# Performance work log

Hardware: AMD Instinct MI355X
Metric: run time of the kernel (lower is better)

Reference implementation:

```python
import jax, jax.numpy as jnp
import numpy as np

HIDDEN = 2048
N_HEADS = 16
HEAD_DIM = HIDDEN // N_HEADS
ROPE_THETA = 10000.0
BSZ, SEQ = 2, 2048
NEG_INF = -1e9


def setup_inputs() -> dict:
    key = jax.random.key(0)
    ks = jax.random.split(key, 5)
    scale = 1.0 / np.sqrt(HIDDEN)
    hidden_states = jax.random.normal(ks[0], (BSZ, SEQ, HIDDEN), dtype=jnp.float32)
    Wq = jax.random.normal(ks[1], (HIDDEN, HIDDEN), dtype=jnp.float32) * scale
    Wk = jax.random.normal(ks[2], (HIDDEN, HIDDEN), dtype=jnp.float32) * scale
    Wv = jax.random.normal(ks[3], (HIDDEN, HIDDEN), dtype=jnp.float32) * scale
    Wo = jax.random.normal(ks[4], (HIDDEN, HIDDEN), dtype=jnp.float32) * scale
    # additive causal mask, [1, 1, S, S]
    causal = jnp.triu(jnp.full((SEQ, SEQ), NEG_INF, dtype=jnp.float32), k=1)
    attention_mask = causal[None, None, :, :]
    position_ids = jnp.arange(SEQ, dtype=jnp.int32)
    return {
        "hidden_states": hidden_states,
        "Wq": Wq, "Wk": Wk, "Wv": Wv, "Wo": Wo,
        "attention_mask": attention_mask,
        "position_ids": position_ids,
    }


def _rotate_half(x):
    half = x.shape[-1] // 2
    return jnp.concatenate((-x[..., half:], x[..., :half]), axis=-1)


def _rope_tables(seq_len, position_ids):
    # inv_freq: [head_dim/2]
    inv_freq = 1.0 / (ROPE_THETA ** (jnp.arange(0, HEAD_DIM, 2, dtype=jnp.float32) / HEAD_DIM))
    t = jnp.arange(seq_len, dtype=jnp.float32)
    freqs = t[:, None] * inv_freq[None, :]              # [S, D/2]
    emb = jnp.concatenate((freqs, freqs), axis=-1)      # [S, D]
    cos = jnp.cos(emb)[position_ids]                    # [S, D]
    sin = jnp.sin(emb)[position_ids]
    return cos, sin


def reference(hidden_states, Wq, Wk, Wv, Wo, attention_mask, position_ids):
    b, s, h = hidden_states.shape
    def proj(W):
        return (hidden_states @ W.T).reshape(b, s, N_HEADS, HEAD_DIM).transpose(0, 2, 1, 3)
    q = proj(Wq)  # [B, H, S, D]
    k = proj(Wk)
    v = proj(Wv)
    cos, sin = _rope_tables(s, position_ids)            # [S, D], broadcasts over B,H
    q = q * cos + _rotate_half(q) * sin
    k = k * cos + _rotate_half(k) * sin
    scores = jnp.einsum('bhqd,bhkd->bhqk', q, k) / np.sqrt(HEAD_DIM)
    scores = scores + attention_mask
    w = jax.nn.softmax(scores, axis=-1)
    out = jnp.einsum('bhqk,bhkd->bhqd', w, v)           # [B, H, S, D]
    out = out.transpose(0, 2, 1, 3).reshape(b, s, h)
    return out @ Wo.T
```

## Files before the change

kernel.cpp:

```cpp
#include <hip/hip_runtime.h>
#include <cstdint>
#include <cstddef>

typedef __bf16 bf16;
typedef __bf16 bf16x4 __attribute__((ext_vector_type(4)));
typedef __bf16 bf16x8 __attribute__((ext_vector_type(8)));
typedef float  f32x4  __attribute__((ext_vector_type(4)));

#define HIDDEN 2048
#define NHEADS 16
#define HDIM   128
#define BSZ    2
#define SEQ    2048
#define BS     (BSZ*SEQ)
#define QKW    (2*HIDDEN)

__device__ __forceinline__ void async16(const bf16* g, bf16* l) {
    __builtin_amdgcn_global_load_lds(
        (const __attribute__((address_space(1))) unsigned int*)g,
        (__attribute__((address_space(3))) unsigned int*)l, 16, 0, 0);
}

__global__ __launch_bounds__(256) void cast_all(const float* __restrict__ hs,
                                                const float* __restrict__ Wq,
                                                const float* __restrict__ Wk,
                                                const float* __restrict__ Wv,
                                                const float* __restrict__ Wo,
                                                bf16* __restrict__ hs_b,
                                                bf16* __restrict__ wqkv,
                                                bf16* __restrict__ wo_b) {
    int i = blockIdx.x * 256 + threadIdx.x;
    const float* src; bf16* dst; int off;
    if (i < 2097152) { src = hs; dst = hs_b; off = i; }
    else {
        int j = i - 2097152;
        int r = j >> 20;
        off = j & 1048575;
        if      (r == 0) { src = Wq; dst = wqkv; }
        else if (r == 1) { src = Wk; dst = wqkv + (size_t)4194304; }
        else if (r == 2) { src = Wv; dst = wqkv + (size_t)8388608; }
        else             { src = Wo; dst = wo_b; }
    }
    const float4 v = ((const float4*)src)[off];
    bf16x4 o;
    o.x = (bf16)v.x; o.y = (bf16)v.y; o.z = (bf16)v.z; o.w = (bf16)v.w;
    ((bf16x4*)dst)[off] = o;
}

__global__ __launch_bounds__(256) void rope_table(const int* __restrict__ pos,
                                                  float2* __restrict__ tab) {
    int i = blockIdx.x * 256 + threadIdx.x;
    int s = i >> 6, p = i & 63;
    float t = (float)pos[s];
    float inv = expf(-(float)(2 * p) * (9.2103403719761836f / 128.0f));
    float sn, cs;
    sincosf(t * inv, &sn, &cs);
    tab[i] = make_float2(cs, sn);
}

__global__ __launch_bounds__(256) void gemm_qkv(const bf16* __restrict__ A,
                                                const bf16* __restrict__ Bt,
                                                const float2* __restrict__ tab,
                                                bf16* __restrict__ qk,
                                                bf16* __restrict__ vtb) {
    __shared__ bf16 Als[128 * 32];
    __shared__ bf16 Bls[128 * 32];
    const int K    = HIDDEN;
    const int tid  = threadIdx.x;
    const int lane = tid & 63;
    const int w    = tid >> 6;
    const int l15  = lane & 15;
    const int quad = lane >> 4;
    const int mTile = blockIdx.y * 128;
    const int nTile = blockIdx.x * 128;
    const int wm = (w >> 1) * 64;
    const int wv = w & 1;

    f32x4 acc[4][4];
#pragma unroll
    for (int i = 0; i < 4; ++i)
#pragma unroll
        for (int j = 0; j < 4; ++j) acc[i][j] = (f32x4){0.f, 0.f, 0.f, 0.f};

    const bf16* gA = A + (size_t)(mTile + w * 32 + (lane >> 2)) * K + (lane & 3) * 8;
    const bf16* gB = Bt + (size_t)(nTile + w * 32 + (lane >> 2)) * K + (lane & 3) * 8;
    bf16* lA = Als + w * 1024;
    bf16* lB = Bls + w * 1024;

    for (int k0 = 0; k0 < K; k0 += 32) {
        async16(gA + k0,          lA);
        async16(gA + 16 * K + k0, lA + 512);
        async16(gB + k0,          lB);
        async16(gB + 16 * K + k0, lB + 512);
        __syncthreads();

        bf16x8 af[4], bfr[4];
#pragma unroll
        for (int mi = 0; mi < 4; ++mi)
            af[mi] = *(const bf16x8*)(Als + (wm + mi * 16 + l15) * 32 + quad * 8);
#pragma unroll
        for (int ni = 0; ni < 4; ++ni) {
            int co = wv * 32 + (ni & 1) * 16 + (ni >> 1) * 64;
            bfr[ni] = *(const bf16x8*)(Bls + (co + l15) * 32 + quad * 8);
        }
#pragma unroll
        for (int mi = 0; mi < 4; ++mi)
#pragma unroll
            for (int ni = 0; ni < 4; ++ni)
                acc[mi][ni] = __builtin_amdgcn_mfma_f32_16x16x32_bf16(
                    af[mi], bfr[ni], acc[mi][ni], 0, 0, 0);
        __syncthreads();
    }

    if (nTile < QKW) {
#pragma unroll
        for (int mi = 0; mi < 4; ++mi)
#pragma unroll
            for (int r = 0; r < 4; ++r) {
                int row = mTile + wm + mi * 16 + quad * 4 + r;
                int s   = row & (SEQ - 1);
                float2 t0 = tab[s * 64 + wv * 32 + l15];
                float2 t1 = tab[s * 64 + wv * 32 + 16 + l15];
                size_t rb = (size_t)row * QKW + nTile + wv * 32 + l15;
                float lo0 = acc[mi][0][r], hi0 = acc[mi][2][r];
                float lo1 = acc[mi][1][r], hi1 = acc[mi][3][r];
                qk[rb]      = (bf16)(lo0 * t0.x - hi0 * t0.y);
                qk[rb + 64] = (bf16)(hi0 * t0.x + lo0 * t0.y);
                qk[rb + 16] = (bf16)(lo1 * t1.x - hi1 * t1.y);
                qk[rb + 80] = (bf16)(hi1 * t1.x + lo1 * t1.y);
            }
    } else {
#pragma unroll
        for (int mi = 0; mi < 4; ++mi)
#pragma unroll
            for (int ni = 0; ni < 4; ++ni) {
                int col_v = (nTile - QKW) + wv * 32 + (ni & 1) * 16 + (ni >> 1) * 64 + l15;
                int row0  = mTile + wm + mi * 16 + quad * 4;
                bf16x4 pk;
#pragma unroll
                for (int r = 0; r < 4; ++r) pk[r] = (bf16)acc[mi][ni][r];
                *(bf16x4*)(vtb + (size_t)col_v * BS + row0) = pk;
            }
    }
}

template <typename OutT>
__global__ __launch_bounds__(256) void gemm_bt(const bf16* __restrict__ A,
                                               const bf16* __restrict__ Bt,
                                               OutT* __restrict__ C,
                                               int M, int N, int K) {
    __shared__ bf16 Als[128 * 32];
    __shared__ bf16 Bls[128 * 32];
    const int tid  = threadIdx.x;
    const int lane = tid & 63;
    const int w    = tid >> 6;
    const int l15  = lane & 15;
    const int quad = lane >> 4;
    const int mTile = blockIdx.y * 128;
    const int nTile = blockIdx.x * 128;
    const int wm = (w >> 1) * 64;
    const int wn = (w & 1) * 64;

    f32x4 acc[4][4];
#pragma unroll
    for (int i = 0; i < 4; ++i)
#pragma unroll
        for (int j = 0; j < 4; ++j) acc[i][j] = (f32x4){0.f, 0.f, 0.f, 0.f};

    const bf16* gA = A + (size_t)(mTile + w * 32 + (lane >> 2)) * K + (lane & 3) * 8;
    const bf16* gB = Bt + (size_t)(nTile + w * 32 + (lane >> 2)) * K + (lane & 3) * 8;
    bf16* lA = Als + w * 1024;
    bf16* lB = Bls + w * 1024;

    for (int k0 = 0; k0 < K; k0 += 32) {
        async16(gA + k0,          lA);
        async16(gA + 16 * K + k0, lA + 512);
        async16(gB + k0,          lB);
        async16(gB + 16 * K + k0, lB + 512);
        __syncthreads();

        bf16x8 af[4], bfr[4];
#pragma unroll
        for (int mi = 0; mi < 4; ++mi)
            af[mi] = *(const bf16x8*)(Als + (wm + mi * 16 + l15) * 32 + quad * 8);
#pragma unroll
        for (int ni = 0; ni < 4; ++ni)
            bfr[ni] = *(const bf16x8*)(Bls + (wn + ni * 16 + l15) * 32 + quad * 8);
#pragma unroll
        for (int mi = 0; mi < 4; ++mi)
#pragma unroll
            for (int ni = 0; ni < 4; ++ni)
                acc[mi][ni] = __builtin_amdgcn_mfma_f32_16x16x32_bf16(
                    af[mi], bfr[ni], acc[mi][ni], 0, 0, 0);
        __syncthreads();
    }

#pragma unroll
    for (int mi = 0; mi < 4; ++mi)
#pragma unroll
        for (int ni = 0; ni < 4; ++ni)
#pragma unroll
            for (int r = 0; r < 4; ++r) {
                int row = mTile + wm + mi * 16 + quad * 4 + r;
                int col = nTile + wn + ni * 16 + l15;
                C[(size_t)row * N + col] = (OutT)acc[mi][ni][r];
            }
}

__global__ __launch_bounds__(256) void attn_kernel(const bf16* __restrict__ qk,
                                                   const bf16* __restrict__ vt,
                                                   bf16* __restrict__ ao) {
    __shared__ bf16 Kls[64 * 128];
    __shared__ bf16 Vls[128 * 64];
    __shared__ bf16 Pls[4 * 16 * 64];

    const int tid  = threadIdx.x;
    const int lane = tid & 63;
    const int w    = tid >> 6;
    const int l15  = lane & 15;
    const int quad = lane >> 4;
    const int l7   = lane & 7;
    const int bid  = blockIdx.x;
    const int qt   = 31 - (bid >> 5);
    const int bh   = bid & 31;
    const int b    = bh >> 4;
    const int h    = bh & 15;
    const int qbase = qt * 64;
    const size_t seq0 = (size_t)b * SEQ;

    bf16x8 qf[4];
    {
        const bf16* qp = qk + (seq0 + qbase + w * 16 + l15) * QKW + h * HDIM + quad * 8;
#pragma unroll
        for (int ks = 0; ks < 4; ++ks) qf[ks] = *(const bf16x8*)(qp + ks * 32);
    }

    f32x4 o[8];
#pragma unroll
    for (int i = 0; i < 8; ++i) o[i] = (f32x4){0.f, 0.f, 0.f, 0.f};
    float m_r[4] = {-3e38f, -3e38f, -3e38f, -3e38f};
    float l_r[4] = {0.f, 0.f, 0.f, 0.f};

    const int krow = lane >> 4;
    const int kp   = lane & 15;
    const int vrow = lane >> 3;
    const int vp   = lane & 7;
    const int sw   = l15 & 7;

    for (int t = 0; t <= qt; ++t) {
        const int kb = t * 64;
#pragma unroll
        for (int i = 0; i < 4; ++i) {
            int j = w * 16 + i * 4 + krow;
            int c = (kp & 8) | ((kp & 7) ^ (j & 7));
            async16(qk + (seq0 + kb + j) * QKW + HIDDEN + h * HDIM + c * 8,
                    Kls + (w * 4 + i) * 512);
        }
#pragma unroll
        for (int i = 0; i < 4; ++i) {
            int d = w * 32 + i * 8 + vrow;
            int c = vp ^ (d & 7);
            async16(vt + (size_t)(h * HDIM + d) * (size_t)BS + seq0 + kb + c * 8,
                    Vls + (w * 4 + i) * 512);
        }
        __syncthreads();

        f32x4 sa[4];
#pragma unroll
        for (int ni = 0; ni < 4; ++ni) sa[ni] = (f32x4){0.f, 0.f, 0.f, 0.f};
#pragma unroll
        for (int ni = 0; ni < 4; ++ni)
#pragma unroll
            for (int ks = 0; ks < 4; ++ks) {
                bf16x8 kf = *(const bf16x8*)(Kls + (ni * 16 + l15) * 128 +
                                             (((ks * 4 + quad) ^ sw) << 3));
                sa[ni] = __builtin_amdgcn_mfma_f32_16x16x32_bf16(qf[ks], kf, sa[ni], 0, 0, 0);
            }

        const float scale = 0.08838834764831845f * 1.4426950408889634f;
        float rmax[4] = {-3e38f, -3e38f, -3e38f, -3e38f};
        const bool diag = (t == qt);
#pragma unroll
        for (int ni = 0; ni < 4; ++ni) {
            int jg = kb + ni * 16 + l15;
#pragma unroll
            for (int r = 0; r < 4; ++r) {
                float sv = sa[ni][r] * scale;
                if (diag) {
                    int qg = qbase + w * 16 + quad * 4 + r;
                    if (jg > qg) sv = -1e30f;
                }
                sa[ni][r] = sv;
                rmax[r] = fmaxf(rmax[r], sv);
            }
        }
#pragma unroll
        for (int off = 1; off < 16; off <<= 1)
#pragma unroll
            for (int r = 0; r < 4; ++r) rmax[r] = fmaxf(rmax[r], __shfl_xor(rmax[r], off));

        float alpha[4];
#pragma unroll
        for (int r = 0; r < 4; ++r) {
            float mn = fmaxf(m_r[r], rmax[r]);
            alpha[r] = exp2f(m_r[r] - mn);
            m_r[r] = mn;
        }
        float rsum[4];
#pragma unroll
        for (int ni = 0; ni < 4; ++ni)
#pragma unroll
            for (int r = 0; r < 4; ++r) sa[ni][r] = exp2f(sa[ni][r] - m_r[r]);
#pragma unroll
        for (int r = 0; r < 4; ++r) rsum[r] = sa[0][r] + sa[1][r] + sa[2][r] + sa[3][r];
#pragma unroll
        for (int off = 1; off < 16; off <<= 1)
#pragma unroll
            for (int r = 0; r < 4; ++r) rsum[r] += __shfl_xor(rsum[r], off);
#pragma unroll
        for (int r = 0; r < 4; ++r) l_r[r] = l_r[r] * alpha[r] + rsum[r];

        bool needscale = (alpha[0] != 1.f) | (alpha[1] != 1.f) |
                         (alpha[2] != 1.f) | (alpha[3] != 1.f);
        if (__ballot(needscale) != 0ull) {
#pragma unroll
            for (int n2 = 0; n2 < 8; ++n2)
#pragma unroll
                for (int r = 0; r < 4; ++r) o[n2][r] *= alpha[r];
        }

        bf16* pw = Pls + w * 1024;
#pragma unroll
        for (int ni = 0; ni < 4; ++ni)
#pragma unroll
            for (int r = 0; r < 4; ++r) {
                int row = quad * 4 + r;
                int cc  = ni * 2 + (l15 >> 3);
                pw[row * 64 + (((cc ^ (row & 7)) << 3) | l7)] = (bf16)sa[ni][r];
            }
        bf16x8 pf0 = *(const bf16x8*)(pw + l15 * 64 + (((quad    ) ^ sw) << 3));
        bf16x8 pf1 = *(const bf16x8*)(pw + l15 * 64 + (((quad + 4) ^ sw) << 3));

#pragma unroll
        for (int n2 = 0; n2 < 8; ++n2) {
            bf16x8 vf0 = *(const bf16x8*)(Vls + (n2 * 16 + l15) * 64 + (((quad    ) ^ sw) << 3));
            bf16x8 vf1 = *(const bf16x8*)(Vls + (n2 * 16 + l15) * 64 + (((quad + 4) ^ sw) << 3));
            o[n2] = __builtin_amdgcn_mfma_f32_16x16x32_bf16(pf0, vf0, o[n2], 0, 0, 0);
            o[n2] = __builtin_amdgcn_mfma_f32_16x16x32_bf16(pf1, vf1, o[n2], 0, 0, 0);
        }
        __syncthreads();
    }

#pragma unroll
    for (int r = 0; r < 4; ++r) l_r[r] = 1.0f / l_r[r];
    bf16* op = ao + (seq0 + qbase + w * 16 + quad * 4) * HIDDEN + h * HDIM + l15;
#pragma unroll
    for (int n2 = 0; n2 < 8; ++n2)
#pragma unroll
        for (int r = 0; r < 4; ++r)
            op[(size_t)r * HIDDEN + n2 * 16] = (bf16)(o[n2][r] * l_r[r]);
}

extern "C" void kernel_launch(void* const* d_in, const int* in_sizes, int n_in,
                              void* d_out, int out_size, void* d_ws, size_t ws_size,
                              hipStream_t stream) {
    const float* hs = (const float*)d_in[0];
    const float* Wq = (const float*)d_in[1];
    const float* Wk = (const float*)d_in[2];
    const float* Wv = (const float*)d_in[3];
    const float* Wo = (const float*)d_in[4];
    const int* pos  = (const int*)d_in[6];
    float* out = (float*)d_out;

    bf16* hs_b = (bf16*)d_ws;
    bf16* wqkv = hs_b + (size_t)8388608;
    bf16* wo_b = wqkv + (size_t)12582912;
    bf16* qkb  = wo_b + (size_t)4194304;
    bf16* vtb  = qkb + (size_t)16777216;
    bf16* ao   = vtb + (size_t)8388608;
    float2* tab = (float2*)ao;

    cast_all<<<24576, 256, 0, stream>>>(hs, Wq, Wk, Wv, Wo, hs_b, wqkv, wo_b);
    rope_table<<<512, 256, 0, stream>>>(pos, tab);
    gemm_qkv<<<dim3(48, 32), 256, 0, stream>>>(hs_b, wqkv, tab, qkb, vtb);
    attn_kernel<<<1024, 256, 0, stream>>>(qkb, vtb, ao);
    gemm_bt<float><<<dim3(HIDDEN / 128, BS / 128), 256, 0, stream>>>(ao, wo_b, out, BS, HIDDEN, HIDDEN);
}
```

Measured before the change: 418.7 us.

## Compute transposed scores to keep P in registers and fuse rope table into cast

The attention kernel now computes S^T by swapping the MFMA operands, so each lane holds one query row's scores. Softmax then needs only two cross-lane shuffles per reduction, and the P probabilities pass straight from registers into 16x16x16 MFMAs with V. This removes the LDS round-trip for P and the per-row 4-way softmax bookkeeping, at the cost of using the smaller k=16 MFMA and 8-byte V reads. Separately, the rope table computation is folded into the cast kernel to save one launch.

```diff
diff --git a/kernel.cpp b/kernel.cpp
--- a/kernel.cpp
+++ b/kernel.cpp
@@ -6,6 +6,7 @@
 typedef __bf16 bf16x4 __attribute__((ext_vector_type(4)));
 typedef __bf16 bf16x8 __attribute__((ext_vector_type(8)));
 typedef float  f32x4  __attribute__((ext_vector_type(4)));
+typedef short  s16x4  __attribute__((ext_vector_type(4)));
 
 #define HIDDEN 2048
 #define NHEADS 16
@@ -15,6 +16,8 @@
 #define BS     (BSZ*SEQ)
 #define QKW    (2*HIDDEN)
 
+union b4u { bf16x4 h; s16x4 s; };
+
 __device__ __forceinline__ void async16(const bf16* g, bf16* l) {
     __builtin_amdgcn_global_load_lds(
         (const __attribute__((address_space(1))) unsigned int*)g,
@@ -26,10 +29,22 @@
                                                 const float* __restrict__ Wk,
                                                 const float* __restrict__ Wv,
                                                 const float* __restrict__ Wo,
+                                                const int* __restrict__ pos,
                                                 bf16* __restrict__ hs_b,
                                                 bf16* __restrict__ wqkv,
-                                                bf16* __restrict__ wo_b) {
+                                                bf16* __restrict__ wo_b,
+                                                float2* __restrict__ tab) {
     int i = blockIdx.x * 256 + threadIdx.x;
+    if (i >= 6291456) {
+        int j = i - 6291456;
+        int s = j >> 6, p = j & 63;
+        float t = (float)pos[s];
+        float inv = expf(-(float)(2 * p) * (9.2103403719761836f / 128.0f));
+        float sn, cs;
+        sincosf(t * inv, &sn, &cs);
+        tab[j] = make_float2(cs, sn);
+        return;
+    }
     const float* src; bf16* dst; int off;
     if (i < 2097152) { src = hs; dst = hs_b; off = i; }
     else {
@@ -45,17 +60,6 @@
     bf16x4 o;
     o.x = (bf16)v.x; o.y = (bf16)v.y; o.z = (bf16)v.z; o.w = (bf16)v.w;
     ((bf16x4*)dst)[off] = o;
-}
-
-__global__ __launch_bounds__(256) void rope_table(const int* __restrict__ pos,
-                                                  float2* __restrict__ tab) {
-    int i = blockIdx.x * 256 + threadIdx.x;
-    int s = i >> 6, p = i & 63;
-    float t = (float)pos[s];
-    float inv = expf(-(float)(2 * p) * (9.2103403719761836f / 128.0f));
-    float sn, cs;
-    sincosf(t * inv, &sn, &cs);
-    tab[i] = make_float2(cs, sn);
 }
 
 __global__ __launch_bounds__(256) void gemm_qkv(const bf16* __restrict__ A,
@@ -212,14 +216,12 @@
                                                    bf16* __restrict__ ao) {
     __shared__ bf16 Kls[64 * 128];
     __shared__ bf16 Vls[128 * 64];
-    __shared__ bf16 Pls[4 * 16 * 64];
 
     const int tid  = threadIdx.x;
     const int lane = tid & 63;
     const int w    = tid >> 6;
     const int l15  = lane & 15;
     const int quad = lane >> 4;
-    const int l7   = lane & 7;
     const int bid  = blockIdx.x;
     const int qt   = 31 - (bid >> 5);
     const int bh   = bid & 31;
@@ -238,8 +240,8 @@
     f32x4 o[8];
 #pragma unroll
     for (int i = 0; i < 8; ++i) o[i] = (f32x4){0.f, 0.f, 0.f, 0.f};
-    float m_r[4] = {-3e38f, -3e38f, -3e38f, -3e38f};
-    float l_r[4] = {0.f, 0.f, 0.f, 0.f};
+    float m_s = -3e38f, l_s = 0.f;
+    const int qg = qbase + w * 16 + l15;
 
     const int krow = lane >> 4;
     const int kp   = lane & 15;
@@ -274,91 +276,72 @@
             for (int ks = 0; ks < 4; ++ks) {
                 bf16x8 kf = *(const bf16x8*)(Kls + (ni * 16 + l15) * 128 +
                                              (((ks * 4 + quad) ^ sw) << 3));
-                sa[ni] = __builtin_amdgcn_mfma_f32_16x16x32_bf16(qf[ks], kf, sa[ni], 0, 0, 0);
+                sa[ni] = __builtin_amdgcn_mfma_f32_16x16x32_bf16(kf, qf[ks], sa[ni], 0, 0, 0);
             }
 
         const float scale = 0.08838834764831845f * 1.4426950408889634f;
-        float rmax[4] = {-3e38f, -3e38f, -3e38f, -3e38f};
+        float rmax = -3e38f;
         const bool diag = (t == qt);
 #pragma unroll
-        for (int ni = 0; ni < 4; ++ni) {
-            int jg = kb + ni * 16 + l15;
+        for (int ni = 0; ni < 4; ++ni)
 #pragma unroll
             for (int r = 0; r < 4; ++r) {
                 float sv = sa[ni][r] * scale;
                 if (diag) {
-                    int qg = qbase + w * 16 + quad * 4 + r;
+                    int jg = kb + ni * 16 + quad * 4 + r;
                     if (jg > qg) sv = -1e30f;
                 }
                 sa[ni][r] = sv;
-                rmax[r] = fmaxf(rmax[r], sv);
-            }
+                rmax = fmaxf(rmax, sv);
+            }
+        rmax = fmaxf(rmax, __shfl_xor(rmax, 16));
+        rmax = fmaxf(rmax, __shfl_xor(rmax, 32));
+
+        float mn = fmaxf(m_s, rmax);
+        float alpha = exp2f(m_s - mn);
+        m_s = mn;
+        float rsum = 0.f;
+        b4u pb[4];
+#pragma unroll
+        for (int ni = 0; ni < 4; ++ni)
+#pragma unroll
+            for (int r = 0; r < 4; ++r) {
+                float e = exp2f(sa[ni][r] - mn);
+                rsum += e;
+                pb[ni].h[r] = (bf16)e;
+            }
+        rsum += __shfl_xor(rsum, 16);
+        rsum += __shfl_xor(rsum, 32);
+        l_s = l_s * alpha + rsum;
+
+        if (__ballot(alpha != 1.f) != 0ull) {
+#pragma unroll
+            for (int n2 = 0; n2 < 8; ++n2)
+#pragma unroll
+                for (int r = 0; r < 4; ++r) o[n2][r] *= alpha;
         }
-#pragma unroll
-        for (int off = 1; off < 16; off <<= 1)
-#pragma unroll
-            for (int r = 0; r < 4; ++r) rmax[r] = fmaxf(rmax[r], __shfl_xor(rmax[r], off));
-
-        float alpha[4];
-#pragma unroll
-        for (int r = 0; r < 4; ++r) {
-            float mn = fmaxf(m_r[r], rmax[r]);
-            alpha[r] = exp2f(m_r[r] - mn);
-            m_r[r] = mn;
-        }
-        float rsum[4];
-#pragma unroll
-        for (int ni = 0; ni < 4; ++ni)
-#pragma unroll
-            for (int r = 0; r < 4; ++r) sa[ni][r] = exp2f(sa[ni][r] - m_r[r]);
-#pragma unroll
-        for (int r = 0; r < 4; ++r) rsum[r] = sa[0][r] + sa[1][r] + sa[2][r] + sa[3][r];
-#pragma unroll
-        for (int off = 1; off < 16; off <<= 1)
-#pragma unroll
-            for (int r = 0; r < 4; ++r) rsum[r] += __shfl_xor(rsum[r], off);
-#pragma unroll
-        for (int r = 0; r < 4; ++r) l_r[r] = l_r[r] * alpha[r] + rsum[r];
-
-        bool needscale = (alpha[0] != 1.f) | (alpha[1] != 1.f) |
-                         (alpha[2] != 1.f) | (alpha[3] != 1.f);
-        if (__ballot(needscale) != 0ull) {
-#pragma unroll
-            for (int n2 = 0; n2 < 8; ++n2)
-#pragma unroll
-                for (int r = 0; r < 4; ++r) o[n2][r] *= alpha[r];
-        }
-
-        bf16* pw = Pls + w * 1024;
-#pragma unroll
-        for (int ni = 0; ni < 4; ++ni)
-#pragma unroll
-            for (int r = 0; r < 4; ++r) {
-                int row = quad * 4 + r;
-                int cc  = ni * 2 + (l15 >> 3);
-                pw[row * 64 + (((cc ^ (row & 7)) << 3) | l7)] = (bf16)sa[ni][r];
-            }
-        bf16x8 pf0 = *(const bf16x8*)(pw + l15 * 64 + (((quad    ) ^ sw) << 3));
-        bf16x8 pf1 = *(const bf16x8*)(pw + l15 * 64 + (((quad + 4) ^ sw) << 3));
-
-#pragma unroll
-        for (int n2 = 0; n2 < 8; ++n2) {
-            bf16x8 vf0 = *(const bf16x8*)(Vls + (n2 * 16 + l15) * 64 + (((quad    ) ^ sw) << 3));
-            bf16x8 vf1 = *(const bf16x8*)(Vls + (n2 * 16 + l15) * 64 + (((quad + 4) ^ sw) << 3));
-            o[n2] = __builtin_amdgcn_mfma_f32_16x16x32_bf16(pf0, vf0, o[n2], 0, 0, 0);
-            o[n2] = __builtin_amdgcn_mfma_f32_16x16x32_bf16(pf1, vf1, o[n2], 0, 0, 0);
-        }
-        __syncthreads();
-    }
-
-#pragma unroll
-    for (int r = 0; r < 4; ++r) l_r[r] = 1.0f / l_r[r];
-    bf16* op = ao + (seq0 + qbase + w * 16 + quad * 4) * HIDDEN + h * HDIM + l15;
-#pragma unroll
-    for (int n2 = 0; n2 < 8; ++n2)
-#pragma unroll
-        for (int r = 0; r < 4; ++r)
-            op[(size_t)r * HIDDEN + n2 * 16] = (bf16)(o[n2][r] * l_r[r]);
+
+#pragma unroll
+        for (int n2 = 0; n2 < 8; ++n2)
+#pragma unroll
+            for (int ni = 0; ni < 4; ++ni) {
+                b4u vf;
+                vf.h = *(const bf16x4*)(Vls + (n2 * 16 + l15) * 64 +
+                                        ((((ni * 2 + (quad >> 1)) ^ sw) << 3) + (quad & 1) * 4));
+                o[n2] = __builtin_amdgcn_mfma_f32_16x16x16bf16_1k(vf.s, pb[ni].s, o[n2], 0, 0, 0);
+            }
+        __syncthreads();
+    }
+
+    const float inv = 1.0f / l_s;
+    bf16* op = ao + (seq0 + qg) * HIDDEN + h * HDIM + quad * 4;
+#pragma unroll
+    for (int n2 = 0; n2 < 8; ++n2) {
+        bf16x4 pk;
+#pragma unroll
+        for (int r = 0; r < 4; ++r) pk[r] = (bf16)(o[n2][r] * inv);
+        *(bf16x4*)(op + n2 * 16) = pk;
+    }
 }
 
 extern "C" void kernel_launch(void* const* d_in, const int* in_sizes, int n_in,
@@ -380,8 +363,7 @@
     bf16* ao   = vtb + (size_t)8388608;
     float2* tab = (float2*)ao;
 
-    cast_all<<<24576, 256, 0, stream>>>(hs, Wq, Wk, Wv, Wo, hs_b, wqkv, wo_b);
-    rope_table<<<512, 256, 0, stream>>>(pos, tab);
+    cast_all<<<25088, 256, 0, stream>>>(hs, Wq, Wk, Wv, Wo, pos, hs_b, wqkv, wo_b, tab);
     gemm_qkv<<<dim3(48, 32), 256, 0, stream>>>(hs_b, wqkv, tab, qkb, vtb);
     attn_kernel<<<1024, 256, 0, stream>>>(qkb, vtb, ao);
     gemm_bt<float><<<dim3(HIDDEN / 128, BS / 128), 256, 0, stream>>>(ao, wo_b, out, BS, HIDDEN, HIDDEN);
```

New measurement: 398.8 us. -4.8%, faster.
